# Kernel optimization log

Hardware: AMD Instinct MI355X
Metric: run time of the kernel (lower is better)

Reference implementation:

```python
import jax, jax.numpy as jnp
import numpy as np

B, T_H, T_W, S_H, S_W = 64, 8, 8, 20, 20
DIM, HEADS = 768, 12
L = 2 * T_H * T_W + S_H * S_W  # 528


def setup_inputs() -> dict:
    key = jax.random.key(0)
    ks = jax.random.split(key, 6)
    sd = 0.02
    return {
        "x": jax.random.normal(ks[0], (B, L, DIM), jnp.float32),
        "Wq": jax.random.normal(ks[1], (DIM, DIM), jnp.float32) * sd,
        "Wk": jax.random.normal(ks[2], (DIM, DIM), jnp.float32) * sd,
        "Wv": jax.random.normal(ks[3], (DIM, DIM), jnp.float32) * sd,
        "Wp": jax.random.normal(ks[4], (DIM, DIM), jnp.float32) * sd,
        "bp": jnp.zeros((DIM,), jnp.float32),
        "t_h": T_H, "t_w": T_W, "s_h": S_H, "s_w": S_W,
    }


def _heads(y, h):
    b, t, d = y.shape
    return y.reshape(b, t, h, d // h).transpose(0, 2, 1, 3)  # b h t d


def _merge(y):
    b, h, t, d = y.shape
    return y.transpose(0, 2, 1, 3).reshape(b, t, h * d)


def _attn(q, k, v, scale):
    s = jnp.einsum("bhld,bhtd->bhlt", q, k) * scale
    p = jax.nn.softmax(s, axis=-1)
    return jnp.einsum("bhlt,bhtd->bhld", p, v)


def reference(x, Wq, Wk, Wv, Wp, bp, t_h, t_w, s_h, s_w):
    # forward_conv with default path is identity: q = k = v = x
    dim = Wq.shape[1]
    scale = dim ** (-0.5)  # NOTE: full dim_out, faithful to original
    q = _heads(x @ Wq, HEADS)
    k = _heads(x @ Wk, HEADS)
    v = _heads(x @ Wv, HEADS)
    Lt = t_h * t_w
    q_t, q_ot, q_s = q[:, :, :Lt], q[:, :, Lt:2 * Lt], q[:, :, 2 * Lt:]
    k12 = k[:, :, :2 * Lt]  # template+online keys
    v12 = v[:, :, :2 * Lt]
    x_t = _attn(q_t, k12, v12, scale)
    x_ot = _attn(q_ot, k12, v12, scale)
    x_s = _attn(q_s, k, v, scale)  # search attends to everything
    out = jnp.concatenate([_merge(x_t), _merge(x_ot), _merge(x_s)], axis=1)
    return out @ Wp + bp
```

## Files before the change

### kernel.cpp

```cpp
#include <hip/hip_runtime.h>
#include <stdint.h>

typedef __attribute__((ext_vector_type(8))) short bf16x8;
typedef __attribute__((ext_vector_type(4))) float f32x4;
typedef unsigned short ushort_t;
typedef unsigned int u32;
typedef const __attribute__((address_space(1))) u32* gp1_t;
typedef __attribute__((address_space(3))) u32* lp3_t;

#define MFMA(a,b,c) __builtin_amdgcn_mfma_f32_16x16x32_bf16((a),(b),(c),0,0,0)

static constexpr int BATCH = 64, LQ = 528, DIM = 768, NH = 12, DH = 64;
static constexpr int MTOK = BATCH * LQ;
static constexpr int VTP  = 544;
static constexpr float QSCALE = (float)(0.03608439182435161 * 1.4426950408889634);

__device__ __forceinline__ ushort_t f2bf(float f) {
  u32 u = __float_as_uint(f);
  u = (u + 0x7fffu + ((u >> 16) & 1u)) >> 16;
  return (ushort_t)u;
}
__device__ __forceinline__ u32 pack2(u32 xr, u32 yr) {
  return __builtin_amdgcn_perm(xr, yr, 0x07060302u);
}
__device__ __forceinline__ u32 cvtpk(float a, float b) {
  u32 r;
  asm("v_cvt_pk_bf16_f32 %0, %1, %2" : "=v"(r) : "v"(a), "v"(b));
  return r;
}
__device__ __forceinline__ int swzK(int r) { return (r & 3) | (((r >> 3) & 1) << 2); }
__device__ __forceinline__ int swzV(int d) { return (d >> 2) & 3; }

__global__ __launch_bounds__(256) void k_convert_x(const float* __restrict__ x,
                                                   ushort_t* __restrict__ xb) {
  int i = blockIdx.x * 256 + threadIdx.x;
  float4 v = ((const float4*)x)[i];
  ushort4 o;
  o.x = f2bf(v.x); o.y = f2bf(v.y); o.z = f2bf(v.z); o.w = f2bf(v.w);
  ((ushort4*)xb)[i] = o;
}

__global__ __launch_bounds__(256) void k_convert_w(
    const float* __restrict__ w0, const float* __restrict__ w1,
    const float* __restrict__ w2, const float* __restrict__ w3,
    ushort_t* __restrict__ o0, ushort_t* __restrict__ o1,
    ushort_t* __restrict__ o2, ushort_t* __restrict__ o3) {
  __shared__ ushort_t t[64][65];
  int mid = blockIdx.z;
  const float* src = (mid == 0) ? w0 : (mid == 1) ? w1 : (mid == 2) ? w2 : w3;
  ushort_t* dst = (mid == 0) ? o0 : (mid == 1) ? o1 : (mid == 2) ? o2 : o3;
  int k0 = blockIdx.x * 64, n0 = blockIdx.y * 64;
  int c = threadIdx.x & 63, rr = threadIdx.x >> 6;
#pragma unroll
  for (int p = 0; p < 16; p++) {
    int r = p * 4 + rr;
    t[c][r] = f2bf(src[(size_t)(k0 + r) * DIM + n0 + c]);
  }
  __syncthreads();
#pragma unroll
  for (int p = 0; p < 16; p++) {
    int r = p * 4 + rr;
    dst[(size_t)(n0 + r) * DIM + k0 + c] = t[r][c];
  }
}

__global__ __launch_bounds__(256, 2) void k_gemm_qkv(
    const ushort_t* __restrict__ A, const ushort_t* __restrict__ wq,
    const ushort_t* __restrict__ wk, const ushort_t* __restrict__ wv,
    ushort_t* __restrict__ Qb, ushort_t* __restrict__ Kb, ushort_t* __restrict__ Vtb) {
  const int id = blockIdx.x, xcd = id & 7, s = id >> 3;
  const int mT = xcd * 33 + s / 18, t = s % 18, w = t / 6, nT = t % 6;
  const ushort_t* Bt = (w == 0) ? wq : (w == 1) ? wk : wv;

  __shared__ ushort_t at[128 * 64];
  __shared__ ushort_t bt[128 * 64];
  const int tid = threadIdx.x;
  const int wv_ = tid >> 6, lane = tid & 63;
  const int lane15 = lane & 15, quad = lane >> 4;
  const int mw = (wv_ & 1) * 64, nw = (wv_ >> 1) * 64;

  f32x4 acc[4][4];
#pragma unroll
  for (int i = 0; i < 4; i++)
#pragma unroll
    for (int j = 0; j < 4; j++) acc[i][j] = (f32x4)0.0f;

  const int lrow = lane >> 3;
  const int lchunk = lane & 7;

  for (int kb = 0; kb < 768; kb += 64) {
#pragma unroll
    for (int i = 0; i < 4; i++) {
      int r0 = wv_ * 32 + i * 8;
      int lr = r0 + lrow;
      size_t off = (size_t)(mT * 128 + lr) * 768 + kb + ((lchunk ^ (lr & 7)) << 3);
      __builtin_amdgcn_global_load_lds((gp1_t)(A + off), (lp3_t)(&at[r0 * 64]), 16, 0, 0);
    }
#pragma unroll
    for (int i = 0; i < 4; i++) {
      int r0 = wv_ * 32 + i * 8;
      int lr = r0 + lrow;
      size_t off = (size_t)(nT * 128 + lr) * 768 + kb + ((lchunk ^ (lr & 7)) << 3);
      __builtin_amdgcn_global_load_lds((gp1_t)(Bt + off), (lp3_t)(&bt[r0 * 64]), 16, 0, 0);
    }
    __syncthreads();
#pragma unroll
    for (int h = 0; h < 2; h++) {
      bf16x8 af[4], bf[4];
#pragma unroll
      for (int mi = 0; mi < 4; mi++) {
        int row = mw + mi * 16 + lane15;
        af[mi] = *(const bf16x8*)&at[row * 64 + (((h * 4 + quad) ^ (row & 7)) << 3)];
      }
#pragma unroll
      for (int ni = 0; ni < 4; ni++) {
        int row = nw + ni * 16 + lane15;
        bf[ni] = *(const bf16x8*)&bt[row * 64 + (((h * 4 + quad) ^ (row & 7)) << 3)];
      }
#pragma unroll
      for (int mi = 0; mi < 4; mi++)
#pragma unroll
        for (int ni = 0; ni < 4; ni++)
          acc[mi][ni] = MFMA(af[mi], bf[ni], acc[mi][ni]);
    }
    __syncthreads();
  }

  const float scale = (w == 0) ? QSCALE : 1.0f;
  ushort_t* Cqk = (w == 0) ? Qb : Kb;
#pragma unroll
  for (int mi = 0; mi < 4; mi++) {
#pragma unroll
    for (int r = 0; r < 4; r++) {
      int m = mT * 128 + mw + mi * 16 + quad * 4 + r;
      int b = m / 528, lt = m - b * 528;
#pragma unroll
      for (int ni = 0; ni < 4; ni++) {
        int n = nT * 128 + nw + ni * 16 + lane15;
        float v = acc[mi][ni][r];
        if (w < 2) {
          Cqk[(((size_t)(b * 12 + (n >> 6)) * 528 + lt) << 6) + (n & 63)] = f2bf(v * scale);
        } else {
          Vtb[((size_t)(b * 12 + (n >> 6)) * 64 + (n & 63)) * VTP + lt] = f2bf(v);
        }
      }
    }
  }
}

__global__ __launch_bounds__(256, 2) void k_gemm_out(const ushort_t* __restrict__ A,
                                                     const ushort_t* __restrict__ Bt,
                                                     float* __restrict__ C,
                                                     const float* __restrict__ bias) {
  const int id = blockIdx.x, xcd = id & 7, s = id >> 3;
  const int mT = xcd * 33 + s / 6, nT = s % 6;

  __shared__ ushort_t at[128 * 64];
  __shared__ ushort_t bt[128 * 64];
  const int tid = threadIdx.x;
  const int wv_ = tid >> 6, lane = tid & 63;
  const int lane15 = lane & 15, quad = lane >> 4;
  const int mw = (wv_ & 1) * 64, nw = (wv_ >> 1) * 64;

  f32x4 acc[4][4];
#pragma unroll
  for (int i = 0; i < 4; i++)
#pragma unroll
    for (int j = 0; j < 4; j++) acc[i][j] = (f32x4)0.0f;

  const int lrow = lane >> 3;
  const int lchunk = lane & 7;

  for (int kb = 0; kb < 768; kb += 64) {
#pragma unroll
    for (int i = 0; i < 4; i++) {
      int r0 = wv_ * 32 + i * 8;
      int lr = r0 + lrow;
      int grow = mT * 128 + lr;
      int gk = kb + ((lchunk ^ (lr & 7)) << 3);
      int b = grow / 528, ltk = grow - b * 528;
      size_t off = (((size_t)(b * 12 + (gk >> 6)) * 528 + ltk) << 6) + (gk & 63);
      __builtin_amdgcn_global_load_lds((gp1_t)(A + off), (lp3_t)(&at[r0 * 64]), 16, 0, 0);
    }
#pragma unroll
    for (int i = 0; i < 4; i++) {
      int r0 = wv_ * 32 + i * 8;
      int lr = r0 + lrow;
      size_t off = (size_t)(nT * 128 + lr) * 768 + kb + ((lchunk ^ (lr & 7)) << 3);
      __builtin_amdgcn_global_load_lds((gp1_t)(Bt + off), (lp3_t)(&bt[r0 * 64]), 16, 0, 0);
    }
    __syncthreads();
#pragma unroll
    for (int h = 0; h < 2; h++) {
      bf16x8 af[4], bf[4];
#pragma unroll
      for (int mi = 0; mi < 4; mi++) {
        int row = mw + mi * 16 + lane15;
        af[mi] = *(const bf16x8*)&at[row * 64 + (((h * 4 + quad) ^ (row & 7)) << 3)];
      }
#pragma unroll
      for (int ni = 0; ni < 4; ni++) {
        int row = nw + ni * 16 + lane15;
        bf[ni] = *(const bf16x8*)&bt[row * 64 + (((h * 4 + quad) ^ (row & 7)) << 3)];
      }
#pragma unroll
      for (int mi = 0; mi < 4; mi++)
#pragma unroll
        for (int ni = 0; ni < 4; ni++)
          acc[mi][ni] = MFMA(af[mi], bf[ni], acc[mi][ni]);
    }
    __syncthreads();
  }

#pragma unroll
  for (int mi = 0; mi < 4; mi++) {
#pragma unroll
    for (int r = 0; r < 4; r++) {
      int m = mT * 128 + mw + mi * 16 + quad * 4 + r;
#pragma unroll
      for (int ni = 0; ni < 4; ni++) {
        int n = nT * 128 + nw + ni * 16 + lane15;
        C[(size_t)m * 768 + n] = acc[mi][ni][r] + bias[n];
      }
    }
  }
}

__global__ __launch_bounds__(256, 3) void k_attn(ushort_t* __restrict__ Q,
                                                 const ushort_t* __restrict__ K,
                                                 const ushort_t* __restrict__ Vt) {
  __shared__ ushort_t Ksh[2][32 * 64];
  __shared__ ushort_t Vsh[2][64 * 32];
  const int tid = threadIdx.x;
  const int wv = tid >> 6, lane = tid & 63;
  const int lane15 = lane & 15, quad = lane >> 4;
  const int b = blockIdx.x, xcd = b & 7, slot = b >> 3;
  const int g = slot / 17, r = slot - g * 17;
  const int bh0 = (xcd * 24 + g) * 4;

  bf16x8 ones;
#pragma unroll
  for (int i = 0; i < 8; i++) ones[i] = (short)0x3F80;

  const int krp = ((lane15 >> 2) << 3) + (lane15 & 3);

  if (r < 16) {
    const int sub = r & 3;
    const int bh = bh0 + (r >> 2);
    const bool light = (sub == 3);
    const int rows0 = light ? (wv * 32) : (128 + sub * 128 + wv * 32);
    const int nch = light ? 4 : 17;

    ushort_t* Qb = Q + (size_t)bh * LQ * DH;
    const ushort_t* Kbh = K + (size_t)bh * LQ * DH;
    const ushort_t* Vbh = Vt + (size_t)bh * DH * VTP;

    bf16x8 aq[2][2];
#pragma unroll
    for (int mt = 0; mt < 2; mt++)
#pragma unroll
      for (int h = 0; h < 2; h++)
        aq[mt][h] = *(const bf16x8*)&Qb[(size_t)(rows0 + mt * 16 + lane15) * DH + h * 32 + quad * 8];

    f32x4 o[2][4], sm[2];
#pragma unroll
    for (int mt = 0; mt < 2; mt++) {
      sm[mt] = (f32x4)0.0f;
#pragma unroll
      for (int dt = 0; dt < 4; dt++) o[mt][dt] = (f32x4)0.0f;
    }

    auto stageKV = [&](int buf, int kc) {
      {
        int rr = tid >> 3, u = tid & 7;
        const ushort_t* src = Kbh + (size_t)(kc + rr) * DH + ((u ^ swzK(rr)) << 3);
        __builtin_amdgcn_global_load_lds((gp1_t)src, (lp3_t)&Ksh[buf][(wv * 8) * 64], 16, 0, 0);
      }
      {
        int d = tid >> 2, cc = tid & 3;
        const ushort_t* src = Vbh + (size_t)d * VTP + kc + ((cc ^ swzV(d)) << 3);
        __builtin_amdgcn_global_load_lds((gp1_t)src, (lp3_t)&Vsh[buf][(wv * 16) * 32], 16, 0, 0);
      }
    };

    auto do_chunk = [&](int c, bool domask) {
      const int buf = c & 1;
      bf16x8 kf[2][2], vf[4];
#pragma unroll
      for (int ss = 0; ss < 2; ss++) {
        int kr = krp + ss * 4;
#pragma unroll
        for (int h = 0; h < 2; h++)
          kf[ss][h] = *(const bf16x8*)&Ksh[buf][kr * 64 + (((h * 4 + quad) ^ swzK(kr)) << 3)];
      }
#pragma unroll
      for (int dt = 0; dt < 4; dt++) {
        int d = dt * 16 + lane15;
        vf[dt] = *(const bf16x8*)&Vsh[buf][d * 32 + ((quad ^ swzV(d)) << 3)];
      }
      const bool maskl = domask && (quad >= 2);
#pragma unroll
      for (int mt = 0; mt < 2; mt++) {
        f32x4 c0 = (f32x4)0.0f, c1 = (f32x4)0.0f;
        c0 = MFMA(kf[0][0], aq[mt][0], c0);
        c0 = MFMA(kf[0][1], aq[mt][1], c0);
        c1 = MFMA(kf[1][0], aq[mt][0], c1);
        c1 = MFMA(kf[1][1], aq[mt][1], c1);
        float e[8];
#pragma unroll
        for (int rr = 0; rr < 4; rr++) {
          e[rr]     = exp2f(maskl ? -30.0f : c0[rr]);
          e[4 + rr] = exp2f(maskl ? -30.0f : c1[rr]);
        }
        union { bf16x8 v; u32 w[4]; } pb;
        pb.w[0] = cvtpk(e[0], e[1]);
        pb.w[1] = cvtpk(e[2], e[3]);
        pb.w[2] = cvtpk(e[4], e[5]);
        pb.w[3] = cvtpk(e[6], e[7]);
        sm[mt] = MFMA(ones, pb.v, sm[mt]);
#pragma unroll
        for (int dt = 0; dt < 4; dt++)
          o[mt][dt] = MFMA(vf[dt], pb.v, o[mt][dt]);
      }
    };

    stageKV(0, 0);
    for (int c = 0; c < nch; c++) {
      __syncthreads();
      if (c + 1 < nch) stageKV((c + 1) & 1, (c + 1) * 32);
      if (c == 16) do_chunk(c, true);
      else         do_chunk(c, false);
    }

#pragma unroll
    for (int mt = 0; mt < 2; mt++) {
      float inv = 1.0f / sm[mt][0];
      ushort_t* orow = &Qb[(size_t)(rows0 + mt * 16 + lane15) * DH];
#pragma unroll
      for (int dt = 0; dt < 4; dt++) {
        uint2 st;
        st.x = cvtpk(o[mt][dt][0] * inv, o[mt][dt][1] * inv);
        st.y = cvtpk(o[mt][dt][2] * inv, o[mt][dt][3] * inv);
        *(uint2*)&orow[dt * 16 + quad * 4] = st;
      }
    }
  } else {
    const int bh = bh0 + wv;
    ushort_t* Qb = Q + (size_t)bh * LQ * DH;
    const ushort_t* Kbh = K + (size_t)bh * LQ * DH;
    const ushort_t* Vbh = Vt + (size_t)bh * DH * VTP;

    bf16x8 aq[2];
#pragma unroll
    for (int h = 0; h < 2; h++)
      aq[h] = *(const bf16x8*)&Qb[(size_t)(512 + lane15) * DH + h * 32 + quad * 8];

    f32x4 o[4], sm = (f32x4)0.0f;
#pragma unroll
    for (int dt = 0; dt < 4; dt++) o[dt] = (f32x4)0.0f;

    const ushort_t* kbase = Kbh + (size_t)krp * DH + quad * 8;
    const ushort_t* vbase = Vbh + (size_t)lane15 * VTP + quad * 8;

    for (int kc = 0; kc < 528; kc += 32) {
      bf16x8 kf[2][2], vf[4];
#pragma unroll
      for (int ss = 0; ss < 2; ss++) {
        const ushort_t* p = kbase + (size_t)(kc + ss * 4) * DH;
        kf[ss][0] = *(const bf16x8*)&p[0];
        kf[ss][1] = *(const bf16x8*)&p[32];
      }
#pragma unroll
      for (int dt = 0; dt < 4; dt++)
        vf[dt] = *(const bf16x8*)&vbase[(size_t)dt * 16 * VTP + kc];

      f32x4 c0 = (f32x4)0.0f, c1 = (f32x4)0.0f;
      c0 = MFMA(kf[0][0], aq[0], c0);
      c0 = MFMA(kf[0][1], aq[1], c0);
      c1 = MFMA(kf[1][0], aq[0], c1);
      c1 = MFMA(kf[1][1], aq[1], c1);
      const bool maskl = (kc == 512) && (quad >= 2);
      float e[8];
#pragma unroll
      for (int rr = 0; rr < 4; rr++) {
        e[rr]     = exp2f(maskl ? -30.0f : c0[rr]);
        e[4 + rr] = exp2f(maskl ? -30.0f : c1[rr]);
      }
      union { bf16x8 v; u32 w[4]; } pb;
      pb.w[0] = cvtpk(e[0], e[1]);
      pb.w[1] = cvtpk(e[2], e[3]);
      pb.w[2] = cvtpk(e[4], e[5]);
      pb.w[3] = cvtpk(e[6], e[7]);
      sm = MFMA(ones, pb.v, sm);
#pragma unroll
      for (int dt = 0; dt < 4; dt++)
        o[dt] = MFMA(vf[dt], pb.v, o[dt]);
    }

    float inv = 1.0f / sm[0];
    ushort_t* orow = &Qb[(size_t)(512 + lane15) * DH];
#pragma unroll
    for (int dt = 0; dt < 4; dt++) {
      uint2 st;
      st.x = cvtpk(o[dt][0] * inv, o[dt][1] * inv);
      st.y = cvtpk(o[dt][2] * inv, o[dt][3] * inv);
      *(uint2*)&orow[dt * 16 + quad * 4] = st;
    }
  }
}

extern "C" void kernel_launch(void* const* d_in, const int* in_sizes, int n_in,
                              void* d_out, int out_size, void* d_ws, size_t ws_size,
                              hipStream_t stream) {
  const float* x = (const float*)d_in[0];
  const float* Wq = (const float*)d_in[1];
  const float* Wk = (const float*)d_in[2];
  const float* Wv = (const float*)d_in[3];
  const float* Wp = (const float*)d_in[4];
  const float* bp = (const float*)d_in[5];
  float* out = (float*)d_out;

  char* ws = (char*)d_ws;
  size_t off = 0;
  auto alloc = [&](size_t bytes) {
    void* p = ws + off;
    off += (bytes + 255) & ~(size_t)255;
    return p;
  };
  ushort_t* xb = (ushort_t*)alloc((size_t)MTOK * DIM * 2);
  ushort_t* wtq = (ushort_t*)alloc((size_t)DIM * DIM * 2);
  ushort_t* wtk = (ushort_t*)alloc((size_t)DIM * DIM * 2);
  ushort_t* wtv = (ushort_t*)alloc((size_t)DIM * DIM * 2);
  ushort_t* wtp = (ushort_t*)alloc((size_t)DIM * DIM * 2);
  ushort_t* Qb = (ushort_t*)alloc((size_t)MTOK * DIM * 2);
  ushort_t* Kb = (ushort_t*)alloc((size_t)MTOK * DIM * 2);
  ushort_t* Vtb = (ushort_t*)alloc((size_t)BATCH * NH * DH * VTP * 2);
  (void)ws_size; (void)in_sizes; (void)n_in; (void)out_size;

  k_convert_x<<<25344, 256, 0, stream>>>(x, xb);
  k_convert_w<<<dim3(12, 12, 4), 256, 0, stream>>>(Wq, Wk, Wv, Wp, wtq, wtk, wtv, wtp);
  k_gemm_qkv<<<4752, 256, 0, stream>>>(xb, wtq, wtk, wtv, Qb, Kb, Vtb);
  k_attn<<<3264, 256, 0, stream>>>(Qb, Kb, Vtb);
  k_gemm_out<<<1584, 256, 0, stream>>>(Qb, wtp, out, bp);
}
```

Before: 473.0 us.

## Load K/V straight from global in attention and merge conversion kernels

```diff
diff --git a/kernel.cpp b/kernel.cpp
--- a/kernel.cpp
+++ b/kernel.cpp
@@ -20,36 +20,32 @@
   u = (u + 0x7fffu + ((u >> 16) & 1u)) >> 16;
   return (ushort_t)u;
 }
-__device__ __forceinline__ u32 pack2(u32 xr, u32 yr) {
-  return __builtin_amdgcn_perm(xr, yr, 0x07060302u);
-}
 __device__ __forceinline__ u32 cvtpk(float a, float b) {
   u32 r;
   asm("v_cvt_pk_bf16_f32 %0, %1, %2" : "=v"(r) : "v"(a), "v"(b));
   return r;
 }
-__device__ __forceinline__ int swzK(int r) { return (r & 3) | (((r >> 3) & 1) << 2); }
-__device__ __forceinline__ int swzV(int d) { return (d >> 2) & 3; }
-
-__global__ __launch_bounds__(256) void k_convert_x(const float* __restrict__ x,
-                                                   ushort_t* __restrict__ xb) {
-  int i = blockIdx.x * 256 + threadIdx.x;
-  float4 v = ((const float4*)x)[i];
-  ushort4 o;
-  o.x = f2bf(v.x); o.y = f2bf(v.y); o.z = f2bf(v.z); o.w = f2bf(v.w);
-  ((ushort4*)xb)[i] = o;
-}
-
-__global__ __launch_bounds__(256) void k_convert_w(
+
+__global__ __launch_bounds__(256) void k_convert(
+    const float* __restrict__ x, ushort_t* __restrict__ xb,
     const float* __restrict__ w0, const float* __restrict__ w1,
     const float* __restrict__ w2, const float* __restrict__ w3,
     ushort_t* __restrict__ o0, ushort_t* __restrict__ o1,
     ushort_t* __restrict__ o2, ushort_t* __restrict__ o3) {
   __shared__ ushort_t t[64][65];
-  int mid = blockIdx.z;
+  if (blockIdx.x < 25344) {
+    int i = blockIdx.x * 256 + threadIdx.x;
+    float4 v = ((const float4*)x)[i];
+    ushort4 o;
+    o.x = f2bf(v.x); o.y = f2bf(v.y); o.z = f2bf(v.z); o.w = f2bf(v.w);
+    ((ushort4*)xb)[i] = o;
+    return;
+  }
+  int bid = blockIdx.x - 25344;
+  int kx = bid % 12, ny = (bid / 12) % 12, mid = bid / 144;
   const float* src = (mid == 0) ? w0 : (mid == 1) ? w1 : (mid == 2) ? w2 : w3;
   ushort_t* dst = (mid == 0) ? o0 : (mid == 1) ? o1 : (mid == 2) ? o2 : o3;
-  int k0 = blockIdx.x * 64, n0 = blockIdx.y * 64;
+  int k0 = kx * 64, n0 = ny * 64;
   int c = threadIdx.x & 63, rr = threadIdx.x >> 6;
 #pragma unroll
   for (int p = 0; p < 16; p++) {
@@ -229,8 +225,6 @@
 __global__ __launch_bounds__(256, 3) void k_attn(ushort_t* __restrict__ Q,
                                                  const ushort_t* __restrict__ K,
                                                  const ushort_t* __restrict__ Vt) {
-  __shared__ ushort_t Ksh[2][32 * 64];
-  __shared__ ushort_t Vsh[2][64 * 32];
   const int tid = threadIdx.x;
   const int wv = tid >> 6, lane = tid & 63;
   const int lane15 = lane & 15, quad = lane >> 4;
@@ -249,7 +243,7 @@
     const int bh = bh0 + (r >> 2);
     const bool light = (sub == 3);
     const int rows0 = light ? (wv * 32) : (128 + sub * 128 + wv * 32);
-    const int nch = light ? 4 : 17;
+    const int kend = light ? 128 : 544;
 
     ushort_t* Qb = Q + (size_t)bh * LQ * DH;
     const ushort_t* Kbh = K + (size_t)bh * LQ * DH;
@@ -270,35 +264,22 @@
       for (int dt = 0; dt < 4; dt++) o[mt][dt] = (f32x4)0.0f;
     }
 
-    auto stageKV = [&](int buf, int kc) {
-      {
-        int rr = tid >> 3, u = tid & 7;
-        const ushort_t* src = Kbh + (size_t)(kc + rr) * DH + ((u ^ swzK(rr)) << 3);
-        __builtin_amdgcn_global_load_lds((gp1_t)src, (lp3_t)&Ksh[buf][(wv * 8) * 64], 16, 0, 0);
-      }
-      {
-        int d = tid >> 2, cc = tid & 3;
-        const ushort_t* src = Vbh + (size_t)d * VTP + kc + ((cc ^ swzV(d)) << 3);
-        __builtin_amdgcn_global_load_lds((gp1_t)src, (lp3_t)&Vsh[buf][(wv * 16) * 32], 16, 0, 0);
-      }
-    };
-
-    auto do_chunk = [&](int c, bool domask) {
-      const int buf = c & 1;
+    const ushort_t* kbase = Kbh + (size_t)krp * DH + quad * 8;
+    const ushort_t* vbase = Vbh + (size_t)lane15 * VTP + quad * 8;
+
+    for (int kc = 0; kc < kend; kc += 32) {
       bf16x8 kf[2][2], vf[4];
 #pragma unroll
       for (int ss = 0; ss < 2; ss++) {
-        int kr = krp + ss * 4;
-#pragma unroll
-        for (int h = 0; h < 2; h++)
-          kf[ss][h] = *(const bf16x8*)&Ksh[buf][kr * 64 + (((h * 4 + quad) ^ swzK(kr)) << 3)];
-      }
-#pragma unroll
-      for (int dt = 0; dt < 4; dt++) {
-        int d = dt * 16 + lane15;
-        vf[dt] = *(const bf16x8*)&Vsh[buf][d * 32 + ((quad ^ swzV(d)) << 3)];
-      }
-      const bool maskl = domask && (quad >= 2);
+        const ushort_t* p = kbase + (size_t)(kc + ss * 4) * DH;
+        kf[ss][0] = *(const bf16x8*)&p[0];
+        kf[ss][1] = *(const bf16x8*)&p[32];
+      }
+#pragma unroll
+      for (int dt = 0; dt < 4; dt++)
+        vf[dt] = *(const bf16x8*)&vbase[(size_t)dt * 16 * VTP + kc];
+
+      const bool maskl = (kc == 512) && (quad >= 2);
 #pragma unroll
       for (int mt = 0; mt < 2; mt++) {
         f32x4 c0 = (f32x4)0.0f, c1 = (f32x4)0.0f;
@@ -322,14 +303,6 @@
         for (int dt = 0; dt < 4; dt++)
           o[mt][dt] = MFMA(vf[dt], pb.v, o[mt][dt]);
       }
-    };
-
-    stageKV(0, 0);
-    for (int c = 0; c < nch; c++) {
-      __syncthreads();
-      if (c + 1 < nch) stageKV((c + 1) & 1, (c + 1) * 32);
-      if (c == 16) do_chunk(c, true);
-      else         do_chunk(c, false);
     }
 
 #pragma unroll
@@ -437,8 +410,7 @@
   ushort_t* Vtb = (ushort_t*)alloc((size_t)BATCH * NH * DH * VTP * 2);
   (void)ws_size; (void)in_sizes; (void)n_in; (void)out_size;
 
-  k_convert_x<<<25344, 256, 0, stream>>>(x, xb);
-  k_convert_w<<<dim3(12, 12, 4), 256, 0, stream>>>(Wq, Wk, Wv, Wp, wtq, wtk, wtv, wtp);
+  k_convert<<<25920, 256, 0, stream>>>(x, xb, Wq, Wk, Wv, Wp, wtq, wtk, wtv, wtp);
   k_gemm_qkv<<<4752, 256, 0, stream>>>(xb, wtq, wtk, wtv, Qb, Kb, Vtb);
   k_attn<<<3264, 256, 0, stream>>>(Qb, Kb, Vtb);
   k_gemm_out<<<1584, 256, 0, stream>>>(Qb, wtp, out, bp);
```

New measurement: 578.1 us. 22.2% more time.

## Enlarge QKV GEMM tile to 256x128 with 8 waves and merge convert kernels

Applied to the files above, without the earlier changes.

```diff
diff --git a/kernel.cpp b/kernel.cpp
--- a/kernel.cpp
+++ b/kernel.cpp
@@ -20,9 +20,6 @@
   u = (u + 0x7fffu + ((u >> 16) & 1u)) >> 16;
   return (ushort_t)u;
 }
-__device__ __forceinline__ u32 pack2(u32 xr, u32 yr) {
-  return __builtin_amdgcn_perm(xr, yr, 0x07060302u);
-}
 __device__ __forceinline__ u32 cvtpk(float a, float b) {
   u32 r;
   asm("v_cvt_pk_bf16_f32 %0, %1, %2" : "=v"(r) : "v"(a), "v"(b));
@@ -31,25 +28,26 @@
 __device__ __forceinline__ int swzK(int r) { return (r & 3) | (((r >> 3) & 1) << 2); }
 __device__ __forceinline__ int swzV(int d) { return (d >> 2) & 3; }
 
-__global__ __launch_bounds__(256) void k_convert_x(const float* __restrict__ x,
-                                                   ushort_t* __restrict__ xb) {
-  int i = blockIdx.x * 256 + threadIdx.x;
-  float4 v = ((const float4*)x)[i];
-  ushort4 o;
-  o.x = f2bf(v.x); o.y = f2bf(v.y); o.z = f2bf(v.z); o.w = f2bf(v.w);
-  ((ushort4*)xb)[i] = o;
-}
-
-__global__ __launch_bounds__(256) void k_convert_w(
+__global__ __launch_bounds__(256) void k_convert(
+    const float* __restrict__ x, ushort_t* __restrict__ xb,
     const float* __restrict__ w0, const float* __restrict__ w1,
     const float* __restrict__ w2, const float* __restrict__ w3,
     ushort_t* __restrict__ o0, ushort_t* __restrict__ o1,
     ushort_t* __restrict__ o2, ushort_t* __restrict__ o3) {
   __shared__ ushort_t t[64][65];
-  int mid = blockIdx.z;
+  if (blockIdx.x < 25344) {
+    int i = blockIdx.x * 256 + threadIdx.x;
+    float4 v = ((const float4*)x)[i];
+    ushort4 o;
+    o.x = f2bf(v.x); o.y = f2bf(v.y); o.z = f2bf(v.z); o.w = f2bf(v.w);
+    ((ushort4*)xb)[i] = o;
+    return;
+  }
+  int bid = blockIdx.x - 25344;
+  int kx = bid % 12, ny = (bid / 12) % 12, mid = bid / 144;
   const float* src = (mid == 0) ? w0 : (mid == 1) ? w1 : (mid == 2) ? w2 : w3;
   ushort_t* dst = (mid == 0) ? o0 : (mid == 1) ? o1 : (mid == 2) ? o2 : o3;
-  int k0 = blockIdx.x * 64, n0 = blockIdx.y * 64;
+  int k0 = kx * 64, n0 = ny * 64;
   int c = threadIdx.x & 63, rr = threadIdx.x >> 6;
 #pragma unroll
   for (int p = 0; p < 16; p++) {
@@ -64,20 +62,22 @@
   }
 }
 
-__global__ __launch_bounds__(256, 2) void k_gemm_qkv(
+__global__ __launch_bounds__(512, 2) void k_gemm_qkv(
     const ushort_t* __restrict__ A, const ushort_t* __restrict__ wq,
     const ushort_t* __restrict__ wk, const ushort_t* __restrict__ wv,
     ushort_t* __restrict__ Qb, ushort_t* __restrict__ Kb, ushort_t* __restrict__ Vtb) {
-  const int id = blockIdx.x, xcd = id & 7, s = id >> 3;
-  const int mT = xcd * 33 + s / 18, t = s % 18, w = t / 6, nT = t % 6;
+  const int orig = blockIdx.x, xcd = orig & 7, s = orig >> 3;
+  const int wgid = xcd * 297 + s;
+  const int mT = wgid / 18, t = wgid % 18;
+  const int w = t / 6, nT = t % 6;
   const ushort_t* Bt = (w == 0) ? wq : (w == 1) ? wk : wv;
 
-  __shared__ ushort_t at[128 * 64];
+  __shared__ ushort_t at[256 * 64];
   __shared__ ushort_t bt[128 * 64];
   const int tid = threadIdx.x;
-  const int wv_ = tid >> 6, lane = tid & 63;
+  const int wid = tid >> 6, lane = tid & 63;
   const int lane15 = lane & 15, quad = lane >> 4;
-  const int mw = (wv_ & 1) * 64, nw = (wv_ >> 1) * 64;
+  const int wm = wid & 3, wn = wid >> 2;
 
   f32x4 acc[4][4];
 #pragma unroll
@@ -91,14 +91,14 @@
   for (int kb = 0; kb < 768; kb += 64) {
 #pragma unroll
     for (int i = 0; i < 4; i++) {
-      int r0 = wv_ * 32 + i * 8;
+      int r0 = i * 64 + wid * 8;
       int lr = r0 + lrow;
-      size_t off = (size_t)(mT * 128 + lr) * 768 + kb + ((lchunk ^ (lr & 7)) << 3);
+      size_t off = (size_t)(mT * 256 + lr) * 768 + kb + ((lchunk ^ (lr & 7)) << 3);
       __builtin_amdgcn_global_load_lds((gp1_t)(A + off), (lp3_t)(&at[r0 * 64]), 16, 0, 0);
     }
 #pragma unroll
-    for (int i = 0; i < 4; i++) {
-      int r0 = wv_ * 32 + i * 8;
+    for (int i = 0; i < 2; i++) {
+      int r0 = i * 64 + wid * 8;
       int lr = r0 + lrow;
       size_t off = (size_t)(nT * 128 + lr) * 768 + kb + ((lchunk ^ (lr & 7)) << 3);
       __builtin_amdgcn_global_load_lds((gp1_t)(Bt + off), (lp3_t)(&bt[r0 * 64]), 16, 0, 0);
@@ -109,12 +109,12 @@
       bf16x8 af[4], bf[4];
 #pragma unroll
       for (int mi = 0; mi < 4; mi++) {
-        int row = mw + mi * 16 + lane15;
+        int row = wm * 64 + mi * 16 + lane15;
         af[mi] = *(const bf16x8*)&at[row * 64 + (((h * 4 + quad) ^ (row & 7)) << 3)];
       }
 #pragma unroll
       for (int ni = 0; ni < 4; ni++) {
-        int row = nw + ni * 16 + lane15;
+        int row = wn * 64 + ni * 16 + lane15;
         bf[ni] = *(const bf16x8*)&bt[row * 64 + (((h * 4 + quad) ^ (row & 7)) << 3)];
       }
 #pragma unroll
@@ -132,11 +132,11 @@
   for (int mi = 0; mi < 4; mi++) {
 #pragma unroll
     for (int r = 0; r < 4; r++) {
-      int m = mT * 128 + mw + mi * 16 + quad * 4 + r;
+      int m = mT * 256 + wm * 64 + mi * 16 + quad * 4 + r;
       int b = m / 528, lt = m - b * 528;
 #pragma unroll
       for (int ni = 0; ni < 4; ni++) {
-        int n = nT * 128 + nw + ni * 16 + lane15;
+        int n = nT * 128 + wn * 64 + ni * 16 + lane15;
         float v = acc[mi][ni][r];
         if (w < 2) {
           Cqk[(((size_t)(b * 12 + (n >> 6)) * 528 + lt) << 6) + (n & 63)] = f2bf(v * scale);
@@ -437,9 +437,8 @@
   ushort_t* Vtb = (ushort_t*)alloc((size_t)BATCH * NH * DH * VTP * 2);
   (void)ws_size; (void)in_sizes; (void)n_in; (void)out_size;
 
-  k_convert_x<<<25344, 256, 0, stream>>>(x, xb);
-  k_convert_w<<<dim3(12, 12, 4), 256, 0, stream>>>(Wq, Wk, Wv, Wp, wtq, wtk, wtv, wtp);
-  k_gemm_qkv<<<4752, 256, 0, stream>>>(xb, wtq, wtk, wtv, Qb, Kb, Vtb);
+  k_convert<<<25920, 256, 0, stream>>>(x, xb, Wq, Wk, Wv, Wp, wtq, wtk, wtv, wtp);
+  k_gemm_qkv<<<2376, 512, 0, stream>>>(xb, wtq, wtk, wtv, Qb, Kb, Vtb);
   k_attn<<<3264, 256, 0, stream>>>(Qb, Kb, Vtb);
   k_gemm_out<<<1584, 256, 0, stream>>>(Qb, wtp, out, bp);
 }
```

Result: slower. 582.0 us (+23.0%).

## Fuse Q, K and V projections into one block sharing the A tile

Applied to the files above, without the earlier changes.

```diff
diff --git a/kernel.cpp b/kernel.cpp
--- a/kernel.cpp
+++ b/kernel.cpp
@@ -19,9 +19,6 @@
   u32 u = __float_as_uint(f);
   u = (u + 0x7fffu + ((u >> 16) & 1u)) >> 16;
   return (ushort_t)u;
-}
-__device__ __forceinline__ u32 pack2(u32 xr, u32 yr) {
-  return __builtin_amdgcn_perm(xr, yr, 0x07060302u);
 }
 __device__ __forceinline__ u32 cvtpk(float a, float b) {
   u32 r;
@@ -69,21 +66,23 @@
     const ushort_t* __restrict__ wk, const ushort_t* __restrict__ wv,
     ushort_t* __restrict__ Qb, ushort_t* __restrict__ Kb, ushort_t* __restrict__ Vtb) {
   const int id = blockIdx.x, xcd = id & 7, s = id >> 3;
-  const int mT = xcd * 33 + s / 18, t = s % 18, w = t / 6, nT = t % 6;
-  const ushort_t* Bt = (w == 0) ? wq : (w == 1) ? wk : wv;
+  const int wgid = xcd * 198 + s;
+  const int mT = wgid / 6, nT = wgid % 6;
 
   __shared__ ushort_t at[128 * 64];
-  __shared__ ushort_t bt[128 * 64];
+  __shared__ ushort_t bt[3][128 * 64];
   const int tid = threadIdx.x;
   const int wv_ = tid >> 6, lane = tid & 63;
   const int lane15 = lane & 15, quad = lane >> 4;
   const int mw = (wv_ & 1) * 64, nw = (wv_ >> 1) * 64;
 
-  f32x4 acc[4][4];
-#pragma unroll
-  for (int i = 0; i < 4; i++)
-#pragma unroll
-    for (int j = 0; j < 4; j++) acc[i][j] = (f32x4)0.0f;
+  f32x4 acc[3][4][4];
+#pragma unroll
+  for (int w = 0; w < 3; w++)
+#pragma unroll
+    for (int i = 0; i < 4; i++)
+#pragma unroll
+      for (int j = 0; j < 4; j++) acc[w][i][j] = (f32x4)0.0f;
 
   const int lrow = lane >> 3;
   const int lchunk = lane & 7;
@@ -97,51 +96,62 @@
       __builtin_amdgcn_global_load_lds((gp1_t)(A + off), (lp3_t)(&at[r0 * 64]), 16, 0, 0);
     }
 #pragma unroll
-    for (int i = 0; i < 4; i++) {
-      int r0 = wv_ * 32 + i * 8;
-      int lr = r0 + lrow;
-      size_t off = (size_t)(nT * 128 + lr) * 768 + kb + ((lchunk ^ (lr & 7)) << 3);
-      __builtin_amdgcn_global_load_lds((gp1_t)(Bt + off), (lp3_t)(&bt[r0 * 64]), 16, 0, 0);
+    for (int w = 0; w < 3; w++) {
+      const ushort_t* Bt = (w == 0) ? wq : (w == 1) ? wk : wv;
+#pragma unroll
+      for (int i = 0; i < 4; i++) {
+        int r0 = wv_ * 32 + i * 8;
+        int lr = r0 + lrow;
+        size_t off = (size_t)(nT * 128 + lr) * 768 + kb + ((lchunk ^ (lr & 7)) << 3);
+        __builtin_amdgcn_global_load_lds((gp1_t)(Bt + off), (lp3_t)(&bt[w][r0 * 64]), 16, 0, 0);
+      }
     }
     __syncthreads();
 #pragma unroll
     for (int h = 0; h < 2; h++) {
-      bf16x8 af[4], bf[4];
+      bf16x8 af[4];
 #pragma unroll
       for (int mi = 0; mi < 4; mi++) {
         int row = mw + mi * 16 + lane15;
         af[mi] = *(const bf16x8*)&at[row * 64 + (((h * 4 + quad) ^ (row & 7)) << 3)];
       }
 #pragma unroll
-      for (int ni = 0; ni < 4; ni++) {
-        int row = nw + ni * 16 + lane15;
-        bf[ni] = *(const bf16x8*)&bt[row * 64 + (((h * 4 + quad) ^ (row & 7)) << 3)];
-      }
-#pragma unroll
-      for (int mi = 0; mi < 4; mi++)
-#pragma unroll
-        for (int ni = 0; ni < 4; ni++)
-          acc[mi][ni] = MFMA(af[mi], bf[ni], acc[mi][ni]);
+      for (int w = 0; w < 3; w++) {
+        bf16x8 bf[4];
+#pragma unroll
+        for (int ni = 0; ni < 4; ni++) {
+          int row = nw + ni * 16 + lane15;
+          bf[ni] = *(const bf16x8*)&bt[w][row * 64 + (((h * 4 + quad) ^ (row & 7)) << 3)];
+        }
+#pragma unroll
+        for (int mi = 0; mi < 4; mi++)
+#pragma unroll
+          for (int ni = 0; ni < 4; ni++)
+            acc[w][mi][ni] = MFMA(af[mi], bf[ni], acc[w][mi][ni]);
+      }
     }
     __syncthreads();
   }
 
-  const float scale = (w == 0) ? QSCALE : 1.0f;
-  ushort_t* Cqk = (w == 0) ? Qb : Kb;
-#pragma unroll
-  for (int mi = 0; mi < 4; mi++) {
-#pragma unroll
-    for (int r = 0; r < 4; r++) {
-      int m = mT * 128 + mw + mi * 16 + quad * 4 + r;
-      int b = m / 528, lt = m - b * 528;
-#pragma unroll
-      for (int ni = 0; ni < 4; ni++) {
-        int n = nT * 128 + nw + ni * 16 + lane15;
-        float v = acc[mi][ni][r];
-        if (w < 2) {
-          Cqk[(((size_t)(b * 12 + (n >> 6)) * 528 + lt) << 6) + (n & 63)] = f2bf(v * scale);
-        } else {
-          Vtb[((size_t)(b * 12 + (n >> 6)) * 64 + (n & 63)) * VTP + lt] = f2bf(v);
+#pragma unroll
+  for (int w = 0; w < 3; w++) {
+    const float scale = (w == 0) ? QSCALE : 1.0f;
+    ushort_t* Cqk = (w == 0) ? Qb : Kb;
+#pragma unroll
+    for (int mi = 0; mi < 4; mi++) {
+#pragma unroll
+      for (int r = 0; r < 4; r++) {
+        int m = mT * 128 + mw + mi * 16 + quad * 4 + r;
+        int b = m / 528, lt = m - b * 528;
+#pragma unroll
+        for (int ni = 0; ni < 4; ni++) {
+          int n = nT * 128 + nw + ni * 16 + lane15;
+          float v = acc[w][mi][ni][r];
+          if (w < 2) {
+            Cqk[(((size_t)(b * 12 + (n >> 6)) * 528 + lt) << 6) + (n & 63)] = f2bf(v * scale);
+          } else {
+            Vtb[((size_t)(b * 12 + (n >> 6)) * 64 + (n & 63)) * VTP + lt] = f2bf(v);
+          }
         }
       }
     }
@@ -439,7 +449,7 @@
 
   k_convert_x<<<25344, 256, 0, stream>>>(x, xb);
   k_convert_w<<<dim3(12, 12, 4), 256, 0, stream>>>(Wq, Wk, Wv, Wp, wtq, wtk, wtv, wtp);
-  k_gemm_qkv<<<4752, 256, 0, stream>>>(xb, wtq, wtk, wtv, Qb, Kb, Vtb);
+  k_gemm_qkv<<<1584, 256, 0, stream>>>(xb, wtq, wtk, wtv, Qb, Kb, Vtb);
   k_attn<<<3264, 256, 0, stream>>>(Qb, Kb, Vtb);
   k_gemm_out<<<1584, 256, 0, stream>>>(Qb, wtp, out, bp);
 }
```

After: 585.0 us. +23.7%, slower.
